# Kernel tuning notes

Measured on AMD Instinct MI355X. Metric: run time of the kernel, lower is better.

## Reference

```python
import jax, jax.numpy as jnp
import numpy as np

RANGE, SHIFT = 0.4, 0.1

def bilerp(plane, gx, gy):
    """torch.grid_sample(mode='bilinear', padding_mode='zeros', align_corners=True).
    plane: [C, H, W]; gx, gy: [P] normalized coords in [-1, 1] (gx->W, gy->H).
    Returns [P, C]."""
    C, H, W = plane.shape
    ix = (gx + 1.0) * 0.5 * (W - 1)
    iy = (gy + 1.0) * 0.5 * (H - 1)
    ix0 = jnp.floor(ix)
    iy0 = jnp.floor(iy)
    wx1 = ix - ix0
    wx0 = 1.0 - wx1
    wy1 = iy - iy0
    wy0 = 1.0 - wy1

    def gather(iyf, ixf):
        yi = iyf.astype(jnp.int32)
        xi = ixf.astype(jnp.int32)
        valid = (yi >= 0) & (yi < H) & (xi >= 0) & (xi < W)
        yc = jnp.clip(yi, 0, H - 1)
        xc = jnp.clip(xi, 0, W - 1)
        v = plane[:, yc, xc]  # [C, P]
        return jnp.where(valid[None, :], v, 0.0)

    out = (gather(iy0, ix0) * (wy0 * wx0)[None, :]
           + gather(iy0, ix0 + 1) * (wy0 * wx1)[None, :]
           + gather(iy0 + 1, ix0) * (wy1 * wx0)[None, :]
           + gather(iy0 + 1, ix0 + 1) * (wy1 * wx1)[None, :])
    return out.T  # [P, C]


def setup_inputs() -> dict:
    key = jax.random.key(0)
    ks = jax.random.split(key, 10)
    Cl, Nl, P = 32, 512, 1000000
    coordinates = jax.random.uniform(ks[0], (1, P, 3), jnp.float32, -1.0, 1.0)
    line_x = jax.random.uniform(ks[1], (Cl, Nl, 1)) * RANGE + SHIFT
    line_y = jax.random.uniform(ks[2], (Cl, Nl, 1)) * RANGE + SHIFT
    line_z = jax.random.uniform(ks[3], (Cl, Nl, 1)) * RANGE + SHIFT
    plane_xy = jax.random.uniform(ks[4], (Cl, Nl, Nl)) * RANGE + SHIFT
    plane_yz = jax.random.uniform(ks[5], (Cl, Nl, Nl)) * RANGE + SHIFT
    plane_xz = jax.random.uniform(ks[6], (Cl, Nl, Nl)) * RANGE + SHIFT
    W1 = jax.random.normal(ks[7], (Cl, 128)) * (1.0 / np.sqrt(Cl))
    b1 = jnp.zeros((128,), jnp.float32)
    W2 = jax.random.normal(ks[8], (128, 1)) * (1.0 / np.sqrt(128))
    b2 = jnp.zeros((1,), jnp.float32)
    return {"coordinates": coordinates, "line_x": line_x, "line_y": line_y,
            "line_z": line_z, "plane_xy": plane_xy, "plane_yz": plane_yz,
            "plane_xz": plane_xz, "W1": W1, "b1": b1, "W2": W2, "b2": b2}


def reference(coordinates, line_x, line_y, line_z, plane_xy, plane_yz, plane_xz,
              W1, b1, W2, b2):
    # batch_size is 1 (original code squeezes dim 0)
    c = coordinates[0]  # [P, 3]
    x, y, z = c[:, 0], c[:, 1], c[:, 2]
    # line sampling: grid = stack([v, v]); grid-x hits W=1 (index 0), grid-y hits H=Nl
    x_embed = bilerp(line_x, x, x)          # [P, Cl]
    y_embed = bilerp(line_y, y, y)
    z_embed = bilerp(line_z, z, z)
    # plane sampling: grid[...,0] -> W axis, grid[...,1] -> H axis
    xy_embed = bilerp(plane_xy, x, y)
    yz_embed = bilerp(plane_yz, y, z)
    xz_embed = bilerp(plane_xz, x, z)
    features = x_embed * yz_embed + y_embed * xz_embed + z_embed * xy_embed
    h = jax.nn.relu(features @ W1 + b1)
    return h @ W2 + b2  # [P, 1]
```

## Files before the change

kernel.cpp:

```cpp
#include <hip/hip_runtime.h>
#include <hip/hip_fp16.h>
#include <stdint.h>

#define PLANE_HALVES (512u * 512u * 32u)

typedef _Float16 f16x8 __attribute__((ext_vector_type(8)));
typedef float    f32x4 __attribute__((ext_vector_type(4)));

__global__ __launch_bounds__(256) void tp_planes(
    const float* __restrict__ pxy,
    const float* __restrict__ pyz,
    const float* __restrict__ pxz,
    __half* __restrict__ ws)
{
    __shared__ float tile[32 * 132];
    unsigned bid = blockIdx.x;
    unsigned p   = bid >> 11;
    unsigned rem = bid & 2047u;
    unsigned y   = rem >> 2;
    unsigned xb  = rem & 3u;
    const float* __restrict__ src = (p == 0) ? pxy : (p == 1) ? pyz : pxz;

    unsigned t  = threadIdx.x;
    unsigned c  = t >> 3;
    unsigned xi = t & 7u;
    const float* srow = src + (size_t)c * 262144u + y * 512u + xb * 128u;
#pragma unroll
    for (int i = 0; i < 4; ++i) {
        float4 v = *reinterpret_cast<const float4*>(srow + xi * 4u + i * 32u);
        *reinterpret_cast<float4*>(&tile[c * 132u + xi * 4u + i * 32u]) = v;
    }
    __syncthreads();

    unsigned xw = t >> 1;
    unsigned h  = t & 1u;
    unsigned c0 = h * 16u;
    __half2 o[8];
#pragma unroll
    for (int i = 0; i < 8; ++i) {
        float a = tile[(c0 + 2u * i) * 132u + xw];
        float b = tile[(c0 + 2u * i + 1u) * 132u + xw];
        o[i] = __floats2half2_rn(a, b);
    }
    __half* dst = ws + (size_t)p * PLANE_HALVES
                + (size_t)(y * 512u + xb * 128u + xw) * 32u + c0;
    reinterpret_cast<uint4*>(dst)[0] = reinterpret_cast<const uint4*>(o)[0];
    reinterpret_cast<uint4*>(dst)[1] = reinterpret_cast<const uint4*>(o)[1];
}

__global__ __launch_bounds__(256) void tp_lines_w1(
    const float* __restrict__ lx, const float* __restrict__ ly,
    const float* __restrict__ lz, float* __restrict__ wl,
    const float* __restrict__ W1, __half* __restrict__ w1f)
{
    if (blockIdx.x < 192) {
        int e = blockIdx.x * 256 + threadIdx.x;
        int l = e >> 14;
        int r = e & 16383;
        int h = r >> 5;
        int c = r & 31;
        const float* src = (l == 0) ? lx : (l == 1) ? ly : lz;
        wl[e] = src[c * 512 + h];
    } else {
        int t = threadIdx.x;
#pragma unroll
        for (int i = 0; i < 16; ++i) {
            int idx = t * 16 + i;
            int e  = idx & 7;
            int ln = (idx >> 3) & 63;
            int ch = idx >> 9;
            int k = ((ln >> 4) << 3) + e;
            int n = (ch << 4) + (ln & 15);
            w1f[idx] = __float2half(W1[k * 128 + n]);
        }
    }
}

struct LI { int i0, i1; float w0, w1; };

__device__ inline LI mk(float g) {
    float t = (g + 1.0f) * 0.5f * 511.0f;
    float f = floorf(t);
    LI r;
    r.w1 = t - f;
    r.w0 = 1.0f - r.w1;
    int i0 = (int)f;
    i0 = i0 < 0 ? 0 : (i0 > 511 ? 511 : i0);
    r.i0 = i0;
    r.i1 = i0 < 511 ? i0 + 1 : 511;
    return r;
}

__device__ inline void load8h(const __half* __restrict__ p, float o[8]) {
    uint4 u = *reinterpret_cast<const uint4*>(p);
    __half2 h0 = *reinterpret_cast<__half2*>(&u.x);
    __half2 h1 = *reinterpret_cast<__half2*>(&u.y);
    __half2 h2 = *reinterpret_cast<__half2*>(&u.z);
    __half2 h3 = *reinterpret_cast<__half2*>(&u.w);
    float2 f0 = __half22float2(h0), f1 = __half22float2(h1);
    float2 f2 = __half22float2(h2), f3 = __half22float2(h3);
    o[0] = f0.x; o[1] = f0.y; o[2] = f1.x; o[3] = f1.y;
    o[4] = f2.x; o[5] = f2.y; o[6] = f3.x; o[7] = f3.y;
}

__device__ inline void bilerp8(const __half* __restrict__ plane,
                               const LI& Hi, const LI& Wi, int c0, float o[8]) {
    float w00 = Hi.w0 * Wi.w0, w01 = Hi.w0 * Wi.w1;
    float w10 = Hi.w1 * Wi.w0, w11 = Hi.w1 * Wi.w1;
    const __half* b00 = plane + ((size_t)(Hi.i0 * 512 + Wi.i0) * 32 + c0);
    const __half* b01 = plane + ((size_t)(Hi.i0 * 512 + Wi.i1) * 32 + c0);
    const __half* b10 = plane + ((size_t)(Hi.i1 * 512 + Wi.i0) * 32 + c0);
    const __half* b11 = plane + ((size_t)(Hi.i1 * 512 + Wi.i1) * 32 + c0);
    float v00[8], v01[8], v10[8], v11[8];
    load8h(b00, v00); load8h(b01, v01); load8h(b10, v10); load8h(b11, v11);
#pragma unroll
    for (int i = 0; i < 8; ++i)
        o[i] = v00[i] * w00 + v01[i] * w01 + v10[i] * w10 + v11[i] * w11;
}

__device__ inline void lerp8(const float* __restrict__ line,
                             const LI& L, int c0, float o[8]) {
    const float4* a = reinterpret_cast<const float4*>(line + L.i0 * 32 + c0);
    const float4* b = reinterpret_cast<const float4*>(line + L.i1 * 32 + c0);
    float4 a0 = a[0], a1 = a[1], b0 = b[0], b1 = b[1];
    o[0] = a0.x * L.w0 + b0.x * L.w1;
    o[1] = a0.y * L.w0 + b0.y * L.w1;
    o[2] = a0.z * L.w0 + b0.z * L.w1;
    o[3] = a0.w * L.w0 + b0.w * L.w1;
    o[4] = a1.x * L.w0 + b1.x * L.w1;
    o[5] = a1.y * L.w0 + b1.y * L.w1;
    o[6] = a1.z * L.w0 + b1.z * L.w1;
    o[7] = a1.w * L.w0 + b1.w * L.w1;
}

__global__ __launch_bounds__(256, 2) void tensorf_fused(
    const float* __restrict__ coords,
    const __half* __restrict__ wsp,
    const float* __restrict__ wsl,
    const __half* __restrict__ w1f,
    const float* __restrict__ b1,
    const float* __restrict__ W2,
    const float* __restrict__ b2,
    float* __restrict__ out, int P)
{
    __shared__ __align__(16) _Float16 sW1f[4096];
    __shared__ float sB1[128];
    __shared__ float sW2[128];
    int tid = threadIdx.x;
    reinterpret_cast<uint4*>(sW1f)[tid]       = reinterpret_cast<const uint4*>(w1f)[tid];
    reinterpret_cast<uint4*>(sW1f)[tid + 256] = reinterpret_cast<const uint4*>(w1f)[tid + 256];
    if (tid < 32)
        reinterpret_cast<float4*>(sB1)[tid] = reinterpret_cast<const float4*>(b1)[tid];
    else if (tid < 64)
        reinterpret_cast<float4*>(sW2)[tid - 32] = reinterpret_cast<const float4*>(W2)[tid - 32];
    __syncthreads();

    int lane = tid & 63;
    int wv   = tid >> 6;
    int r    = lane & 15;
    int q    = lane >> 4;
    int c0   = q * 8;
    int base = blockIdx.x * 256 + wv * 64;

    const __half* pXY = wsp;
    const __half* pYZ = wsp + 8388608u;
    const __half* pXZ = wsp + 16777216u;
    const float* lX = wsl;
    const float* lY = wsl + 16384;
    const float* lZ = wsl + 32768;

    f16x8 af[4];
#pragma unroll
    for (int m = 0; m < 4; ++m) {
        int p  = base + m * 16 + r;
        int pc = p < P ? p : P - 1;
        float x = coords[3 * pc + 0];
        float y = coords[3 * pc + 1];
        float z = coords[3 * pc + 2];
        LI ax = mk(x), ay = mk(y), az = mk(z);

        float f[8], pv[8], lv[8];
        bilerp8(pYZ, az, ay, c0, pv);
        lerp8(lX, ax, c0, lv);
#pragma unroll
        for (int i = 0; i < 8; ++i) f[i] = lv[i] * pv[i];

        bilerp8(pXZ, az, ax, c0, pv);
        lerp8(lY, ay, c0, lv);
#pragma unroll
        for (int i = 0; i < 8; ++i) f[i] = fmaf(lv[i], pv[i], f[i]);

        bilerp8(pXY, ay, ax, c0, pv);
        lerp8(lZ, az, c0, lv);
#pragma unroll
        for (int i = 0; i < 8; ++i) f[i] = fmaf(lv[i], pv[i], f[i]);

        f16x8 a;
#pragma unroll
        for (int i = 0; i < 8; ++i) a[i] = (_Float16)f[i];
        af[m] = a;
    }

    float accm[4][4];
#pragma unroll
    for (int m = 0; m < 4; ++m)
#pragma unroll
        for (int t = 0; t < 4; ++t) accm[m][t] = 0.f;

#pragma unroll
    for (int ch = 0; ch < 8; ++ch) {
        f16x8 bf = *reinterpret_cast<const f16x8*>(&sW1f[(ch * 64 + lane) * 8]);
        float bb  = sB1[ch * 16 + r];
        float w2v = sW2[ch * 16 + r];
#pragma unroll
        for (int m = 0; m < 4; ++m) {
            f32x4 cacc = {bb, bb, bb, bb};
            cacc = __builtin_amdgcn_mfma_f32_16x16x32_f16(af[m], bf, cacc, 0, 0, 0);
#pragma unroll
            for (int t = 0; t < 4; ++t) {
                float h = fmaxf(cacc[t], 0.f);
                accm[m][t] = fmaf(h, w2v, accm[m][t]);
            }
        }
    }

#pragma unroll
    for (int m = 0; m < 4; ++m)
#pragma unroll
        for (int t = 0; t < 4; ++t) {
            float v = accm[m][t];
            v += __shfl_xor(v, 1);
            v += __shfl_xor(v, 2);
            v += __shfl_xor(v, 4);
            v += __shfl_xor(v, 8);
            accm[m][t] = v;
        }

    if (r == 0) {
        float b2v = b2[0];
#pragma unroll
        for (int m = 0; m < 4; ++m)
#pragma unroll
            for (int t = 0; t < 4; ++t) {
                int p = base + m * 16 + q * 4 + t;
                if (p < P) out[p] = accm[m][t] + b2v;
            }
    }
}

extern "C" void kernel_launch(void* const* d_in, const int* in_sizes, int n_in,
                              void* d_out, int out_size, void* d_ws, size_t ws_size,
                              hipStream_t stream)
{
    const float* coords   = (const float*)d_in[0];
    const float* line_x   = (const float*)d_in[1];
    const float* line_y   = (const float*)d_in[2];
    const float* line_z   = (const float*)d_in[3];
    const float* plane_xy = (const float*)d_in[4];
    const float* plane_yz = (const float*)d_in[5];
    const float* plane_xz = (const float*)d_in[6];
    const float* W1 = (const float*)d_in[7];
    const float* b1 = (const float*)d_in[8];
    const float* W2 = (const float*)d_in[9];
    const float* b2 = (const float*)d_in[10];
    int P = in_sizes[0] / 3;

    size_t planes_b = 3ull * PLANE_HALVES * 2ull;
    size_t lines_b  = 3ull * 512ull * 32ull * 4ull;
    size_t w1f_b    = 4096ull * 2ull;
    if (ws_size < planes_b + lines_b + w1f_b) return;

    __half* wsp = (__half*)d_ws;
    float*  wsl = (float*)((char*)d_ws + planes_b);
    __half* w1f = (__half*)((char*)d_ws + planes_b + lines_b);

    tp_planes<<<6144, 256, 0, stream>>>(plane_xy, plane_yz, plane_xz, wsp);
    tp_lines_w1<<<193, 256, 0, stream>>>(line_x, line_y, line_z, wsl, W1, w1f);

    int grid = (P + 255) / 256;
    tensorf_fused<<<grid, 256, 0, stream>>>(coords, wsp, wsl, w1f, b1, W2, b2,
                                            (float*)d_out, P);
}
```

Baseline: 316.0 us.

## Bucket-sort points by Morton key before fused sampling for gather locality

Adds a counting sort of the sample points into 32^3 Morton-ordered buckets (histogram, single-block scan, atomic scatter), then runs the fused kernel on the sorted point list and writes results back through the stored original indices. It also remaps block IDs so consecutive sorted chunks land on the same XCD, so nearby points share L2. The aim is to cut cache misses on the random plane and line gathers. The cost is three extra kernels, a memset, atomics and an extra 16-byte-per-point buffer, and it only runs when the workspace is large enough.

```diff
diff --git a/kernel.cpp b/kernel.cpp
--- a/kernel.cpp
+++ b/kernel.cpp
@@ -3,6 +3,7 @@
 #include <stdint.h>
 
 #define PLANE_HALVES (512u * 512u * 32u)
+#define NBUCKET 32768
 
 typedef _Float16 f16x8 __attribute__((ext_vector_type(8)));
 typedef float    f32x4 __attribute__((ext_vector_type(4)));
@@ -74,6 +75,74 @@
             w1f[idx] = __float2half(W1[k * 128 + n]);
         }
     }
+}
+
+__device__ inline unsigned expand5(unsigned v) {
+    unsigned e = 0;
+    e |= (v & 1u);
+    e |= (v & 2u)  << 2;
+    e |= (v & 4u)  << 4;
+    e |= (v & 8u)  << 6;
+    e |= (v & 16u) << 8;
+    return e;
+}
+
+__device__ inline unsigned morton_key(float x, float y, float z) {
+    float ux = (x + 1.0f) * 16.0f;
+    float uy = (y + 1.0f) * 16.0f;
+    float uz = (z + 1.0f) * 16.0f;
+    int cx = (int)ux; cx = cx < 0 ? 0 : (cx > 31 ? 31 : cx);
+    int cy = (int)uy; cy = cy < 0 ? 0 : (cy > 31 ? 31 : cy);
+    int cz = (int)uz; cz = cz < 0 ? 0 : (cz > 31 ? 31 : cz);
+    return expand5((unsigned)cx) | (expand5((unsigned)cy) << 1)
+         | (expand5((unsigned)cz) << 2);
+}
+
+__global__ __launch_bounds__(256) void histo_k(
+    const float* __restrict__ coords, unsigned* __restrict__ hist, int P)
+{
+    int p = blockIdx.x * 256 + threadIdx.x;
+    if (p >= P) return;
+    float x = coords[3 * p + 0];
+    float y = coords[3 * p + 1];
+    float z = coords[3 * p + 2];
+    atomicAdd(&hist[morton_key(x, y, z)], 1u);
+}
+
+__global__ __launch_bounds__(1024) void scan_k(unsigned* __restrict__ hist)
+{
+    __shared__ unsigned ps[1024];
+    int t = threadIdx.x;
+    unsigned loc[32];
+    unsigned s = 0;
+#pragma unroll
+    for (int i = 0; i < 32; ++i) { loc[i] = hist[t * 32 + i]; s += loc[i]; }
+    ps[t] = s;
+    __syncthreads();
+    for (int off = 1; off < 1024; off <<= 1) {
+        unsigned v = 0;
+        if (t >= off) v = ps[t - off];
+        __syncthreads();
+        if (t >= off) ps[t] += v;
+        __syncthreads();
+    }
+    unsigned run = ps[t] - s;
+#pragma unroll
+    for (int i = 0; i < 32; ++i) { hist[t * 32 + i] = run; run += loc[i]; }
+}
+
+__global__ __launch_bounds__(256) void scatter_k(
+    const float* __restrict__ coords, unsigned* __restrict__ cursor,
+    float4* __restrict__ sc, int P)
+{
+    int p = blockIdx.x * 256 + threadIdx.x;
+    if (p >= P) return;
+    float x = coords[3 * p + 0];
+    float y = coords[3 * p + 1];
+    float z = coords[3 * p + 2];
+    unsigned pos = atomicAdd(&cursor[morton_key(x, y, z)], 1u);
+    float4 v; v.x = x; v.y = y; v.z = z; v.w = __int_as_float(p);
+    sc[pos] = v;
 }
 
 struct LI { int i0, i1; float w0, w1; };
@@ -133,15 +202,17 @@
     o[7] = a1.w * L.w0 + b1.w * L.w1;
 }
 
+template<bool SORTED>
 __global__ __launch_bounds__(256, 2) void tensorf_fused(
     const float* __restrict__ coords,
+    const float4* __restrict__ sc,
     const __half* __restrict__ wsp,
     const float* __restrict__ wsl,
     const __half* __restrict__ w1f,
     const float* __restrict__ b1,
     const float* __restrict__ W2,
     const float* __restrict__ b2,
-    float* __restrict__ out, int P)
+    float* __restrict__ out, int P, int nwg)
 {
     __shared__ __align__(16) _Float16 sW1f[4096];
     __shared__ float sB1[128];
@@ -155,12 +226,19 @@
         reinterpret_cast<float4*>(sW2)[tid - 32] = reinterpret_cast<const float4*>(W2)[tid - 32];
     __syncthreads();
 
+    int bid = blockIdx.x;
+    if (SORTED) {
+        int qq = nwg >> 3, rr = nwg & 7;
+        int xcd = bid & 7, idx = bid >> 3;
+        bid = (xcd < rr ? xcd * (qq + 1) : rr * (qq + 1) + (xcd - rr) * qq) + idx;
+    }
+
     int lane = tid & 63;
     int wv   = tid >> 6;
     int r    = lane & 15;
     int q    = lane >> 4;
     int c0   = q * 8;
-    int base = blockIdx.x * 256 + wv * 64;
+    int base = bid * 256 + wv * 64;
 
     const __half* pXY = wsp;
     const __half* pYZ = wsp + 8388608u;
@@ -174,9 +252,15 @@
     for (int m = 0; m < 4; ++m) {
         int p  = base + m * 16 + r;
         int pc = p < P ? p : P - 1;
-        float x = coords[3 * pc + 0];
-        float y = coords[3 * pc + 1];
-        float z = coords[3 * pc + 2];
+        float x, y, z;
+        if (SORTED) {
+            float4 v = sc[pc];
+            x = v.x; y = v.y; z = v.z;
+        } else {
+            x = coords[3 * pc + 0];
+            y = coords[3 * pc + 1];
+            z = coords[3 * pc + 2];
+        }
         LI ax = mk(x), ay = mk(y), az = mk(z);
 
         float f[8], pv[8], lv[8];
@@ -238,12 +322,16 @@
 
     if (r == 0) {
         float b2v = b2[0];
+        const float* scf = reinterpret_cast<const float*>(sc);
 #pragma unroll
         for (int m = 0; m < 4; ++m)
 #pragma unroll
             for (int t = 0; t < 4; ++t) {
                 int p = base + m * 16 + q * 4 + t;
-                if (p < P) out[p] = accm[m][t] + b2v;
+                if (p < P) {
+                    int op = SORTED ? __float_as_int(scf[p * 4 + 3]) : p;
+                    out[op] = accm[m][t] + b2v;
+                }
             }
     }
 }
@@ -268,7 +356,11 @@
     size_t planes_b = 3ull * PLANE_HALVES * 2ull;
     size_t lines_b  = 3ull * 512ull * 32ull * 4ull;
     size_t w1f_b    = 4096ull * 2ull;
-    if (ws_size < planes_b + lines_b + w1f_b) return;
+    size_t base_need = planes_b + lines_b + w1f_b;
+    size_t sc_b     = (size_t)P * 16ull;
+    size_t hist_b   = (size_t)NBUCKET * 4ull;
+
+    if (ws_size < base_need) return;
 
     __half* wsp = (__half*)d_ws;
     float*  wsl = (float*)((char*)d_ws + planes_b);
@@ -278,6 +370,20 @@
     tp_lines_w1<<<193, 256, 0, stream>>>(line_x, line_y, line_z, wsl, W1, w1f);
 
     int grid = (P + 255) / 256;
-    tensorf_fused<<<grid, 256, 0, stream>>>(coords, wsp, wsl, w1f, b1, W2, b2,
-                                            (float*)d_out, P);
-}
+    bool sorted = (ws_size >= base_need + sc_b + hist_b);
+
+    if (sorted) {
+        float4*   sc   = (float4*)((char*)d_ws + base_need);
+        unsigned* hist = (unsigned*)((char*)d_ws + base_need + sc_b);
+        hipMemsetAsync(hist, 0, hist_b, stream);
+        histo_k<<<grid, 256, 0, stream>>>(coords, hist, P);
+        scan_k<<<1, 1024, 0, stream>>>(hist);
+        scatter_k<<<grid, 256, 0, stream>>>(coords, hist, sc, P);
+        tensorf_fused<true><<<grid, 256, 0, stream>>>(
+            coords, sc, wsp, wsl, w1f, b1, W2, b2, (float*)d_out, P, grid);
+    } else {
+        tensorf_fused<false><<<grid, 256, 0, stream>>>(
+            coords, (const float4*)nullptr, wsp, wsl, w1f, b1, W2, b2,
+            (float*)d_out, P, grid);
+    }
+}
```

After: 442.8 us. 1.4x slower.

## Pack line neighbor pairs as half2 and pad coordinates to float4

Applied to the files above, without the earlier changes.

The line tables are rebuilt so each entry holds the value at index i and i+1 as a half2 pair. A lerp then needs one 32-byte contiguous load instead of two float loads from different rows. A new pre-pass copies the 3-float coordinates into a padded float4 buffer so the fused kernel can fetch each point with one vector load. The cost is an extra kernel launch plus a 16 MB write and read of coordinates, and line precision drops to fp16.

```diff
diff --git a/kernel.cpp b/kernel.cpp
--- a/kernel.cpp
+++ b/kernel.cpp
@@ -50,7 +50,7 @@
 
 __global__ __launch_bounds__(256) void tp_lines_w1(
     const float* __restrict__ lx, const float* __restrict__ ly,
-    const float* __restrict__ lz, float* __restrict__ wl,
+    const float* __restrict__ lz, __half2* __restrict__ wl2,
     const float* __restrict__ W1, __half* __restrict__ w1f)
 {
     if (blockIdx.x < 192) {
@@ -60,7 +60,9 @@
         int h = r >> 5;
         int c = r & 31;
         const float* src = (l == 0) ? lx : (l == 1) ? ly : lz;
-        wl[e] = src[c * 512 + h];
+        float a = src[c * 512 + h];
+        float b = src[c * 512 + (h < 511 ? h + 1 : h)];
+        wl2[e] = __floats2half2_rn(a, b);
     } else {
         int t = threadIdx.x;
 #pragma unroll
@@ -74,6 +76,19 @@
             w1f[idx] = __float2half(W1[k * 128 + n]);
         }
     }
+}
+
+__global__ __launch_bounds__(256) void tp_coords(
+    const float* __restrict__ coords, float4* __restrict__ c4, int P)
+{
+    int p = blockIdx.x * 256 + threadIdx.x;
+    if (p >= P) return;
+    float4 v;
+    v.x = coords[3 * p + 0];
+    v.y = coords[3 * p + 1];
+    v.z = coords[3 * p + 2];
+    v.w = 0.f;
+    c4[p] = v;
 }
 
 struct LI { int i0, i1; float w0, w1; };
@@ -118,25 +133,24 @@
         o[i] = v00[i] * w00 + v01[i] * w01 + v10[i] * w10 + v11[i] * w11;
 }
 
-__device__ inline void lerp8(const float* __restrict__ line,
-                             const LI& L, int c0, float o[8]) {
-    const float4* a = reinterpret_cast<const float4*>(line + L.i0 * 32 + c0);
-    const float4* b = reinterpret_cast<const float4*>(line + L.i1 * 32 + c0);
-    float4 a0 = a[0], a1 = a[1], b0 = b[0], b1 = b[1];
-    o[0] = a0.x * L.w0 + b0.x * L.w1;
-    o[1] = a0.y * L.w0 + b0.y * L.w1;
-    o[2] = a0.z * L.w0 + b0.z * L.w1;
-    o[3] = a0.w * L.w0 + b0.w * L.w1;
-    o[4] = a1.x * L.w0 + b1.x * L.w1;
-    o[5] = a1.y * L.w0 + b1.y * L.w1;
-    o[6] = a1.z * L.w0 + b1.z * L.w1;
-    o[7] = a1.w * L.w0 + b1.w * L.w1;
+__device__ inline void lerp8_pair(const __half2* __restrict__ line2,
+                                  const LI& L, int c0, float o[8]) {
+    const uint4* pp = reinterpret_cast<const uint4*>(line2 + L.i0 * 32 + c0);
+    uint4 u0 = pp[0], u1 = pp[1];
+    unsigned ua[8] = {u0.x, u0.y, u0.z, u0.w, u1.x, u1.y, u1.z, u1.w};
+#pragma unroll
+    for (int i = 0; i < 8; ++i) {
+        __half2 h = *reinterpret_cast<__half2*>(&ua[i]);
+        float2 f = __half22float2(h);
+        o[i] = f.x * L.w0 + f.y * L.w1;
+    }
 }
 
 __global__ __launch_bounds__(256, 2) void tensorf_fused(
     const float* __restrict__ coords,
+    const float4* __restrict__ c4,
     const __half* __restrict__ wsp,
-    const float* __restrict__ wsl,
+    const __half2* __restrict__ wl2,
     const __half* __restrict__ w1f,
     const float* __restrict__ b1,
     const float* __restrict__ W2,
@@ -165,33 +179,39 @@
     const __half* pXY = wsp;
     const __half* pYZ = wsp + 8388608u;
     const __half* pXZ = wsp + 16777216u;
-    const float* lX = wsl;
-    const float* lY = wsl + 16384;
-    const float* lZ = wsl + 32768;
+    const __half2* lX2 = wl2;
+    const __half2* lY2 = wl2 + 16384;
+    const __half2* lZ2 = wl2 + 32768;
 
     f16x8 af[4];
 #pragma unroll
     for (int m = 0; m < 4; ++m) {
         int p  = base + m * 16 + r;
         int pc = p < P ? p : P - 1;
-        float x = coords[3 * pc + 0];
-        float y = coords[3 * pc + 1];
-        float z = coords[3 * pc + 2];
+        float x, y, z;
+        if (c4) {
+            float4 cv = c4[pc];
+            x = cv.x; y = cv.y; z = cv.z;
+        } else {
+            x = coords[3 * pc + 0];
+            y = coords[3 * pc + 1];
+            z = coords[3 * pc + 2];
+        }
         LI ax = mk(x), ay = mk(y), az = mk(z);
 
         float f[8], pv[8], lv[8];
         bilerp8(pYZ, az, ay, c0, pv);
-        lerp8(lX, ax, c0, lv);
+        lerp8_pair(lX2, ax, c0, lv);
 #pragma unroll
         for (int i = 0; i < 8; ++i) f[i] = lv[i] * pv[i];
 
         bilerp8(pXZ, az, ax, c0, pv);
-        lerp8(lY, ay, c0, lv);
+        lerp8_pair(lY2, ay, c0, lv);
 #pragma unroll
         for (int i = 0; i < 8; ++i) f[i] = fmaf(lv[i], pv[i], f[i]);
 
         bilerp8(pXY, ay, ax, c0, pv);
-        lerp8(lZ, az, c0, lv);
+        lerp8_pair(lZ2, az, c0, lv);
 #pragma unroll
         for (int i = 0; i < 8; ++i) f[i] = fmaf(lv[i], pv[i], f[i]);
 
@@ -266,18 +286,25 @@
     int P = in_sizes[0] / 3;
 
     size_t planes_b = 3ull * PLANE_HALVES * 2ull;
-    size_t lines_b  = 3ull * 512ull * 32ull * 4ull;
     size_t w1f_b    = 4096ull * 2ull;
-    if (ws_size < planes_b + lines_b + w1f_b) return;
-
-    __half* wsp = (__half*)d_ws;
-    float*  wsl = (float*)((char*)d_ws + planes_b);
-    __half* w1f = (__half*)((char*)d_ws + planes_b + lines_b);
+    size_t wl2_b    = 3ull * 512ull * 32ull * 4ull;
+    size_t base_need = planes_b + w1f_b + wl2_b;
+    size_t c4_b     = (size_t)P * 16ull;
+    if (ws_size < base_need) return;
+
+    __half*  wsp = (__half*)d_ws;
+    __half*  w1f = (__half*)((char*)d_ws + planes_b);
+    __half2* wl2 = (__half2*)((char*)d_ws + planes_b + w1f_b);
+    bool use_c4  = (ws_size >= base_need + c4_b);
+    float4*  c4  = use_c4 ? (float4*)((char*)d_ws + base_need) : (float4*)nullptr;
 
     tp_planes<<<6144, 256, 0, stream>>>(plane_xy, plane_yz, plane_xz, wsp);
-    tp_lines_w1<<<193, 256, 0, stream>>>(line_x, line_y, line_z, wsl, W1, w1f);
+    tp_lines_w1<<<193, 256, 0, stream>>>(line_x, line_y, line_z, wl2, W1, w1f);
 
     int grid = (P + 255) / 256;
-    tensorf_fused<<<grid, 256, 0, stream>>>(coords, wsp, wsl, w1f, b1, W2, b2,
+    if (use_c4)
+        tp_coords<<<grid, 256, 0, stream>>>(coords, c4, P);
+
+    tensorf_fused<<<grid, 256, 0, stream>>>(coords, c4, wsp, wl2, w1f, b1, W2, b2,
                                             (float*)d_out, P);
 }
```

New measurement: 351.5 us. +11.2%, slower.
